# Kernel optimization log

Measured on AMD Instinct MI355X. Metric: run time of the kernel, lower is better.

The kernel has to match this reference:

```python
import jax, jax.numpy as jnp
import numpy as np

B, S, D_IN, D_OUT = 8, 2048, 512, 512

def setup_inputs() -> dict:
    key = jax.random.key(0)
    ks = jax.random.split(key, 10)
    s = 1.0 / np.sqrt(D_IN)
    return {
        "Q": jax.random.normal(ks[0], (B, S, D_IN), jnp.float32),
        "K": jax.random.normal(ks[1], (B, S, D_IN), jnp.float32),
        "V": jax.random.normal(ks[2], (B, S, D_IN), jnp.float32),
        "attn_mask": jax.random.normal(ks[3], (B, S, S), jnp.float32),
        "Wq": jax.random.normal(ks[4], (D_IN, D_OUT), jnp.float32) * s,
        "bq": jnp.zeros((D_OUT,), jnp.float32),
        "Wk": jax.random.normal(ks[5], (D_IN, D_OUT), jnp.float32) * s,
        "bk": jnp.zeros((D_OUT,), jnp.float32),
        "Wv": jax.random.normal(ks[6], (D_IN, D_OUT), jnp.float32) * s,
        "bv": jnp.zeros((D_OUT,), jnp.float32),
    }

def reference(Q, K, V, attn_mask, Wq, bq, Wk, bk, Wv, bv):
    # separate QKV projections
    q_s = jnp.einsum('bsd,de->bse', Q, Wq) + bq
    k_s = jnp.einsum('bsd,de->bse', K, Wk) + bk
    v_s = jnp.einsum('bsd,de->bse', V, Wv) + bv
    # scaled dot-product; note: source scales by sqrt(d_in)
    scale = 1.0 / np.sqrt(Q.shape[-1]).astype(np.float32)
    scores = jnp.einsum('bqe,bke->bqk', q_s, k_s) * scale + attn_mask
    attn = jax.nn.softmax(scores, axis=-1)
    return jnp.einsum('bqk,bke->bqe', attn, v_s)
```

## Files before the change

### kernel.cpp

```cpp
#include <hip/hip_runtime.h>


typedef __bf16 bf16x8 __attribute__((ext_vector_type(8)));
typedef float f32x4 __attribute__((ext_vector_type(4)));

__device__ inline unsigned short f2bf(float x) {
  union { float f; unsigned u; } c; c.f = x;
  unsigned u = c.u;
  return (unsigned short)((u + 0x7fffu + ((u >> 16) & 1u)) >> 16);
}

__device__ inline void load_lds16(const void* g, void* lds) {
  __builtin_amdgcn_global_load_lds(
      (__attribute__((address_space(1))) void*)(g),
      (__attribute__((address_space(3))) void*)(lds),
      16, 0, 0);
}

__global__ __launch_bounds__(256) void cvt4(const float4* __restrict__ src,
                                            ushort4* __restrict__ dst, int n4) {
  int i = blockIdx.x * 256 + threadIdx.x;
  if (i < n4) {
    float4 f = src[i];
    ushort4 o;
    o.x = f2bf(f.x); o.y = f2bf(f.y); o.z = f2bf(f.z); o.w = f2bf(f.w);
    dst[i] = o;
  }
}

__global__ void wtrans(const float* __restrict__ W, unsigned short* __restrict__ Wt) {
  __shared__ float t[32][33];
  const int x = threadIdx.x, y = threadIdx.y;
  const int n0 = blockIdx.x * 32, k0 = blockIdx.y * 32;
#pragma unroll
  for (int j = 0; j < 32; j += 8) t[y + j][x] = W[(size_t)(k0 + y + j) * 512 + n0 + x];
  __syncthreads();
#pragma unroll
  for (int j = 0; j < 32; j += 8)
    Wt[(size_t)(n0 + y + j) * 512 + k0 + x] = f2bf(t[x][y + j]);
}

enum { EPI_PROJ = 0, EPI_SCORES = 1, EPI_PV = 2 };

template <int EPI, int BN>
__global__ __launch_bounds__(256) void gemm_bt(
    const unsigned short* __restrict__ A, size_t sA, int lda,
    const unsigned short* __restrict__ B, size_t sB, int ldb,
    void* __restrict__ Cv, size_t sC, int ldc, int K,
    const float* __restrict__ b0, const float* __restrict__ b1,
    const float* __restrict__ b2, unsigned short* __restrict__ VT,
    const float* __restrict__ mask, float scale, float* __restrict__ Lsum) {
  constexpr int NF = BN / 32;
  __shared__ unsigned short As[128 * 64];
  __shared__ unsigned short Bs[BN * 64];

  const int tid = threadIdx.x;
  const int wave = tid >> 6, lane = tid & 63;
  const int z = blockIdx.z;
  const int m0 = blockIdx.y * 128, n0 = blockIdx.x * BN;

  const unsigned short* Ab = A + (size_t)z * sA;
  const unsigned short* Bb = B + (size_t)z * sB;

  const int wr = wave >> 1, wc = wave & 1;
  const int quad = lane >> 4, c16 = lane & 15;
  const int srow8 = lane >> 3;
  const int sslot = ((lane & 7) ^ srow8) * 8;

  f32x4 acc[4][NF] = {};

  if constexpr (EPI == EPI_SCORES) {
    const float* mb = mask + (size_t)z * 2048 * 2048;
    const float invs = 1.0f / scale;
#pragma unroll
    for (int fr = 0; fr < 4; ++fr)
#pragma unroll
      for (int fc = 0; fc < NF; ++fc)
#pragma unroll
        for (int r = 0; r < 4; ++r)
          acc[fr][fc][r] =
              mb[(size_t)(m0 + wr * 64 + fr * 16 + quad * 4 + r) * 2048 +
                 (n0 + wc * (BN / 2) + fc * 16 + c16)] * invs;
  }

  auto stage = [&](int kt) {
#pragma unroll
    for (int i = 0; i < 4; ++i) {
      const int inst = wave * 4 + i;
      const int row = inst * 8 + srow8;
      load_lds16(Ab + (size_t)(m0 + row) * lda + kt + sslot, &As[inst * 512]);
    }
#pragma unroll
    for (int i = 0; i < BN / 32; ++i) {
      const int inst = wave * (BN / 32) + i;
      const int row = inst * 8 + srow8;
      load_lds16(Bb + (size_t)(n0 + row) * ldb + kt + sslot, &Bs[inst * 512]);
    }
  };

  auto compute = [&]() {
#pragma unroll
    for (int ks = 0; ks < 2; ++ks) {
      bf16x8 af[4], bf[NF];
#pragma unroll
      for (int i = 0; i < 4; ++i) {
        const int row = wr * 64 + i * 16 + c16;
        const int slot = (ks * 4 + quad) ^ (row & 7);
        af[i] = *(const bf16x8*)&As[row * 64 + slot * 8];
      }
#pragma unroll
      for (int j = 0; j < NF; ++j) {
        const int row = wc * (BN / 2) + j * 16 + c16;
        const int slot = (ks * 4 + quad) ^ (row & 7);
        bf[j] = *(const bf16x8*)&Bs[row * 64 + slot * 8];
      }
#pragma unroll
      for (int i = 0; i < 4; ++i)
#pragma unroll
        for (int j = 0; j < NF; ++j)
          acc[i][j] = __builtin_amdgcn_mfma_f32_16x16x32_bf16(af[i], bf[j], acc[i][j], 0, 0, 0);
    }
  };

  if constexpr (EPI == EPI_SCORES) {
#pragma unroll
    for (int it = 0; it < 8; ++it) {
      __syncthreads();
      stage(it * 64);
      __syncthreads();
      compute();
    }
  } else {
    for (int kt = 0; kt < K; kt += 64) {
      __syncthreads();
      stage(kt);
      __syncthreads();
      compute();
    }
  }

#pragma unroll
  for (int fr = 0; fr < 4; ++fr) {
    const int rbase = m0 + wr * 64 + fr * 16 + quad * 4;
    if constexpr (EPI == EPI_PROJ) {
#pragma unroll
      for (int fc = 0; fc < NF; ++fc) {
        const int col = n0 + wc * (BN / 2) + fc * 16 + c16;
        const float bias = (z == 0 ? b0 : (z == 1 ? b1 : b2))[col];
        if (z < 2) {
          unsigned short* C = (unsigned short*)Cv + (size_t)z * sC;
#pragma unroll
          for (int r = 0; r < 4; ++r)
            C[(size_t)(rbase + r) * ldc + col] = f2bf(acc[fr][fc][r] + bias);
        } else {
          const int b = rbase >> 11, s = rbase & 2047;
          ushort4 p;
          p.x = f2bf(acc[fr][fc][0] + bias);
          p.y = f2bf(acc[fr][fc][1] + bias);
          p.z = f2bf(acc[fr][fc][2] + bias);
          p.w = f2bf(acc[fr][fc][3] + bias);
          *(ushort4*)(VT + ((size_t)b * 512 + col) * 2048 + s) = p;
        }
      }
    } else if constexpr (EPI == EPI_SCORES) {
      unsigned short* P = (unsigned short*)Cv + (size_t)z * sC;
      float rs[4] = {0.f, 0.f, 0.f, 0.f};
#pragma unroll
      for (int fc = 0; fc < NF; ++fc) {
        const int col = n0 + wc * (BN / 2) + fc * 16 + c16;
#pragma unroll
        for (int r = 0; r < 4; ++r) {
          const float e = __expf(acc[fr][fc][r] * scale);
          P[(size_t)(rbase + r) * ldc + col] = f2bf(e);
          rs[r] += e;
        }
      }
#pragma unroll
      for (int r = 0; r < 4; ++r) {
#pragma unroll
        for (int off = 1; off < 16; off <<= 1) rs[r] += __shfl_xor(rs[r], off);
      }
      if (c16 == 0) {
#pragma unroll
        for (int r = 0; r < 4; ++r)
          atomicAdd(&Lsum[(size_t)z * 2048 + rbase + r], rs[r]);
      }
    } else {
      float* C = (float*)Cv + (size_t)z * sC;
      float inv[4];
#pragma unroll
      for (int r = 0; r < 4; ++r) inv[r] = 1.0f / Lsum[(size_t)z * 2048 + rbase + r];
#pragma unroll
      for (int fc = 0; fc < NF; ++fc) {
        const int col = n0 + wc * (BN / 2) + fc * 16 + c16;
#pragma unroll
        for (int r = 0; r < 4; ++r)
          C[(size_t)(rbase + r) * ldc + col] = acc[fr][fc][r] * inv[r];
      }
    }
  }
}

extern "C" void kernel_launch(void* const* d_in, const int* in_sizes, int n_in,
                              void* d_out, int out_size, void* d_ws, size_t ws_size,
                              hipStream_t stream) {
  const float* Q    = (const float*)d_in[0];
  const float* Kin  = (const float*)d_in[1];
  const float* V    = (const float*)d_in[2];
  const float* mask = (const float*)d_in[3];
  const float* Wq   = (const float*)d_in[4];
  const float* bq   = (const float*)d_in[5];
  const float* Wk   = (const float*)d_in[6];
  const float* bk   = (const float*)d_in[7];
  const float* Wv   = (const float*)d_in[8];
  const float* bv   = (const float*)d_in[9];
  float* out = (float*)d_out;

  const size_t TOKD = (size_t)16384 * 512;

  unsigned short* WT = (unsigned short*)d_ws;
  unsigned short* QS = WT + 3 * 512 * 512;
  unsigned short* KS = QS + TOKD;
  unsigned short* VT = KS + TOKD;
  unsigned short* P  = VT + TOKD;
  float* Lsum = (float*)(P + (size_t)8 * 2048 * 2048);
  unsigned short* QB = (unsigned short*)(Lsum + 16384);

  const float scale = 0.044194173824159216f;

  const int n4 = (int)(TOKD / 4);
  cvt4<<<n4 / 256, 256, 0, stream>>>((const float4*)Q,   (ushort4*)QB, n4);
  cvt4<<<n4 / 256, 256, 0, stream>>>((const float4*)Kin, (ushort4*)(QB + TOKD), n4);
  cvt4<<<n4 / 256, 256, 0, stream>>>((const float4*)V,   (ushort4*)(QB + 2 * TOKD), n4);

  dim3 wtb(32, 8);
  wtrans<<<dim3(16, 16), wtb, 0, stream>>>(Wq, WT);
  wtrans<<<dim3(16, 16), wtb, 0, stream>>>(Wk, WT + 262144);
  wtrans<<<dim3(16, 16), wtb, 0, stream>>>(Wv, WT + 524288);

  hipMemsetAsync(Lsum, 0, 16384 * sizeof(float), stream);

  gemm_bt<EPI_PROJ, 128><<<dim3(4, 128, 3), 256, 0, stream>>>(
      QB, TOKD, 512, WT, 262144, 512, (void*)QS, TOKD, 512, 512,
      bq, bk, bv, VT, nullptr, 0.f, nullptr);

  gemm_bt<EPI_SCORES, 128><<<dim3(16, 16, 8), 256, 0, stream>>>(
      QS, (size_t)2048 * 512, 512,
      KS, (size_t)2048 * 512, 512,
      (void*)P, (size_t)2048 * 2048, 2048, 512,
      nullptr, nullptr, nullptr, nullptr, mask, scale, Lsum);

  gemm_bt<EPI_PV, 64><<<dim3(8, 16, 8), 256, 0, stream>>>(
      P, (size_t)2048 * 2048, 2048,
      VT, (size_t)512 * 2048, 2048,
      (void*)out, (size_t)2048 * 512, 512, 2048,
      nullptr, nullptr, nullptr, nullptr, nullptr, 0.f, Lsum);
}
```

Measured before the change: 465.9 us.

## Use 256-row double-buffered 512-thread GEMM for scores and PV stages

Adds a new gemm256 kernel with 256xBN tiles, 8 waves per block and double-buffered LDS staging, so the next K-tile loads while the current one computes with one barrier per iteration. The scores and PV GEMMs now use it, and the projection GEMM keeps the old kernel with its scores/PV paths removed. Larger tiles raise data reuse per LDS load. They also increase LDS (up to 128KB per block for scores) and register use, and with fewer blocks per grid this can lower occupancy and CU fill.

```diff
diff --git a/kernel.cpp b/kernel.cpp
--- a/kernel.cpp
+++ b/kernel.cpp
@@ -48,8 +48,7 @@
     const unsigned short* __restrict__ B, size_t sB, int ldb,
     void* __restrict__ Cv, size_t sC, int ldc, int K,
     const float* __restrict__ b0, const float* __restrict__ b1,
-    const float* __restrict__ b2, unsigned short* __restrict__ VT,
-    const float* __restrict__ mask, float scale, float* __restrict__ Lsum) {
+    const float* __restrict__ b2, unsigned short* __restrict__ VT) {
   constexpr int NF = BN / 32;
   __shared__ unsigned short As[128 * 64];
   __shared__ unsigned short Bs[BN * 64];
@@ -69,20 +68,6 @@
 
   f32x4 acc[4][NF] = {};
 
-  if constexpr (EPI == EPI_SCORES) {
-    const float* mb = mask + (size_t)z * 2048 * 2048;
-    const float invs = 1.0f / scale;
-#pragma unroll
-    for (int fr = 0; fr < 4; ++fr)
-#pragma unroll
-      for (int fc = 0; fc < NF; ++fc)
-#pragma unroll
-        for (int r = 0; r < 4; ++r)
-          acc[fr][fc][r] =
-              mb[(size_t)(m0 + wr * 64 + fr * 16 + quad * 4 + r) * 2048 +
-                 (n0 + wc * (BN / 2) + fc * 16 + c16)] * invs;
-  }
-
   auto stage = [&](int kt) {
 #pragma unroll
     for (int i = 0; i < 4; ++i) {
@@ -122,52 +107,144 @@
     }
   };
 
-  if constexpr (EPI == EPI_SCORES) {
-#pragma unroll
-    for (int it = 0; it < 8; ++it) {
-      __syncthreads();
-      stage(it * 64);
-      __syncthreads();
-      compute();
-    }
-  } else {
-    for (int kt = 0; kt < K; kt += 64) {
-      __syncthreads();
-      stage(kt);
-      __syncthreads();
-      compute();
-    }
+  for (int kt = 0; kt < K; kt += 64) {
+    __syncthreads();
+    stage(kt);
+    __syncthreads();
+    compute();
   }
 
 #pragma unroll
   for (int fr = 0; fr < 4; ++fr) {
     const int rbase = m0 + wr * 64 + fr * 16 + quad * 4;
-    if constexpr (EPI == EPI_PROJ) {
-#pragma unroll
-      for (int fc = 0; fc < NF; ++fc) {
-        const int col = n0 + wc * (BN / 2) + fc * 16 + c16;
-        const float bias = (z == 0 ? b0 : (z == 1 ? b1 : b2))[col];
-        if (z < 2) {
-          unsigned short* C = (unsigned short*)Cv + (size_t)z * sC;
-#pragma unroll
-          for (int r = 0; r < 4; ++r)
-            C[(size_t)(rbase + r) * ldc + col] = f2bf(acc[fr][fc][r] + bias);
-        } else {
-          const int b = rbase >> 11, s = rbase & 2047;
-          ushort4 p;
-          p.x = f2bf(acc[fr][fc][0] + bias);
-          p.y = f2bf(acc[fr][fc][1] + bias);
-          p.z = f2bf(acc[fr][fc][2] + bias);
-          p.w = f2bf(acc[fr][fc][3] + bias);
-          *(ushort4*)(VT + ((size_t)b * 512 + col) * 2048 + s) = p;
-        }
-      }
-    } else if constexpr (EPI == EPI_SCORES) {
+#pragma unroll
+    for (int fc = 0; fc < NF; ++fc) {
+      const int col = n0 + wc * (BN / 2) + fc * 16 + c16;
+      const float bias = (z == 0 ? b0 : (z == 1 ? b1 : b2))[col];
+      if (z < 2) {
+        unsigned short* C = (unsigned short*)Cv + (size_t)z * sC;
+#pragma unroll
+        for (int r = 0; r < 4; ++r)
+          C[(size_t)(rbase + r) * ldc + col] = f2bf(acc[fr][fc][r] + bias);
+      } else {
+        const int b = rbase >> 11, s = rbase & 2047;
+        ushort4 p;
+        p.x = f2bf(acc[fr][fc][0] + bias);
+        p.y = f2bf(acc[fr][fc][1] + bias);
+        p.z = f2bf(acc[fr][fc][2] + bias);
+        p.w = f2bf(acc[fr][fc][3] + bias);
+        *(ushort4*)(VT + ((size_t)b * 512 + col) * 2048 + s) = p;
+      }
+    }
+  }
+}
+
+template <int EPI, int BN>
+__global__ __launch_bounds__(512, 2) void gemm256(
+    const unsigned short* __restrict__ A, size_t sA, int lda,
+    const unsigned short* __restrict__ B, size_t sB, int ldb,
+    void* __restrict__ Cv, size_t sC, int ldc, int K,
+    const float* __restrict__ mask, float scale, float* __restrict__ Lsum) {
+  constexpr int WCOL = BN / 4;
+  constexpr int NF = WCOL / 16;
+  __shared__ unsigned short As[2][256 * 64];
+  __shared__ unsigned short Bs[2][BN * 64];
+
+  const int tid = threadIdx.x;
+  const int wave = tid >> 6, lane = tid & 63;
+  const int z = blockIdx.z;
+  const int m0 = blockIdx.y * 256, n0 = blockIdx.x * BN;
+
+  const unsigned short* Ab = A + (size_t)z * sA;
+  const unsigned short* Bb = B + (size_t)z * sB;
+
+  const int wr = wave >> 2, wc = wave & 3;
+  const int quad = lane >> 4, c16 = lane & 15;
+  const int srow8 = lane >> 3;
+  const int sslot = ((lane & 7) ^ srow8) * 8;
+
+  f32x4 acc[8][NF] = {};
+
+  if constexpr (EPI == EPI_SCORES) {
+    const float* mb = mask + (size_t)z * 2048 * 2048;
+    const float invs = 1.0f / scale;
+#pragma unroll
+    for (int fr = 0; fr < 8; ++fr)
+#pragma unroll
+      for (int fc = 0; fc < NF; ++fc)
+#pragma unroll
+        for (int r = 0; r < 4; ++r)
+          acc[fr][fc][r] =
+              mb[(size_t)(m0 + wr * 128 + fr * 16 + quad * 4 + r) * 2048 +
+                 (n0 + wc * WCOL + fc * 16 + c16)] * invs;
+  }
+
+  auto stage = [&](int kt, int b) {
+#pragma unroll
+    for (int i = 0; i < 4; ++i) {
+      const int inst = wave * 4 + i;
+      const int row = inst * 8 + srow8;
+      load_lds16(Ab + (size_t)(m0 + row) * lda + kt + sslot, &As[b][inst * 512]);
+    }
+#pragma unroll
+    for (int i = 0; i < BN / 64; ++i) {
+      const int inst = wave * (BN / 64) + i;
+      const int row = inst * 8 + srow8;
+      load_lds16(Bb + (size_t)(n0 + row) * ldb + kt + sslot, &Bs[b][inst * 512]);
+    }
+  };
+
+  auto compute = [&](int b) {
+#pragma unroll
+    for (int ks = 0; ks < 2; ++ks) {
+      bf16x8 af[8], bf[NF];
+#pragma unroll
+      for (int i = 0; i < 8; ++i) {
+        const int row = wr * 128 + i * 16 + c16;
+        const int slot = (ks * 4 + quad) ^ (row & 7);
+        af[i] = *(const bf16x8*)&As[b][row * 64 + slot * 8];
+      }
+#pragma unroll
+      for (int j = 0; j < NF; ++j) {
+        const int row = wc * WCOL + j * 16 + c16;
+        const int slot = (ks * 4 + quad) ^ (row & 7);
+        bf[j] = *(const bf16x8*)&Bs[b][row * 64 + slot * 8];
+      }
+#pragma unroll
+      for (int i = 0; i < 8; ++i)
+#pragma unroll
+        for (int j = 0; j < NF; ++j)
+          acc[i][j] = __builtin_amdgcn_mfma_f32_16x16x32_bf16(af[i], bf[j], acc[i][j], 0, 0, 0);
+    }
+  };
+
+  stage(0, 0);
+  __syncthreads();
+  if constexpr (EPI == EPI_SCORES) {
+#pragma unroll
+    for (int t = 0; t < 8; ++t) {
+      if (t < 7) stage((t + 1) * 64, (t + 1) & 1);
+      compute(t & 1);
+      __syncthreads();
+    }
+  } else {
+    const int nt = K >> 6;
+    for (int t = 0; t < nt; ++t) {
+      if (t + 1 < nt) stage((t + 1) * 64, (t + 1) & 1);
+      compute(t & 1);
+      __syncthreads();
+    }
+  }
+
+#pragma unroll
+  for (int fr = 0; fr < 8; ++fr) {
+    const int rbase = m0 + wr * 128 + fr * 16 + quad * 4;
+    if constexpr (EPI == EPI_SCORES) {
       unsigned short* P = (unsigned short*)Cv + (size_t)z * sC;
       float rs[4] = {0.f, 0.f, 0.f, 0.f};
 #pragma unroll
       for (int fc = 0; fc < NF; ++fc) {
-        const int col = n0 + wc * (BN / 2) + fc * 16 + c16;
+        const int col = n0 + wc * WCOL + fc * 16 + c16;
 #pragma unroll
         for (int r = 0; r < 4; ++r) {
           const float e = __expf(acc[fr][fc][r] * scale);
@@ -192,7 +269,7 @@
       for (int r = 0; r < 4; ++r) inv[r] = 1.0f / Lsum[(size_t)z * 2048 + rbase + r];
 #pragma unroll
       for (int fc = 0; fc < NF; ++fc) {
-        const int col = n0 + wc * (BN / 2) + fc * 16 + c16;
+        const int col = n0 + wc * WCOL + fc * 16 + c16;
 #pragma unroll
         for (int r = 0; r < 4; ++r)
           C[(size_t)(rbase + r) * ldc + col] = acc[fr][fc][r] * inv[r];
@@ -242,17 +319,17 @@
 
   gemm_bt<EPI_PROJ, 128><<<dim3(4, 128, 3), 256, 0, stream>>>(
       QB, TOKD, 512, WT, 262144, 512, (void*)QS, TOKD, 512, 512,
-      bq, bk, bv, VT, nullptr, 0.f, nullptr);
-
-  gemm_bt<EPI_SCORES, 128><<<dim3(16, 16, 8), 256, 0, stream>>>(
+      bq, bk, bv, VT);
+
+  gemm256<EPI_SCORES, 256><<<dim3(8, 8, 8), 512, 0, stream>>>(
       QS, (size_t)2048 * 512, 512,
       KS, (size_t)2048 * 512, 512,
       (void*)P, (size_t)2048 * 2048, 2048, 512,
-      nullptr, nullptr, nullptr, nullptr, mask, scale, Lsum);
-
-  gemm_bt<EPI_PV, 64><<<dim3(8, 16, 8), 256, 0, stream>>>(
+      mask, scale, Lsum);
+
+  gemm256<EPI_PV, 128><<<dim3(4, 8, 8), 512, 0, stream>>>(
       P, (size_t)2048 * 2048, 2048,
       VT, (size_t)512 * 2048, 2048,
       (void*)out, (size_t)2048 * 512, 512, 2048,
-      nullptr, nullptr, nullptr, nullptr, nullptr, 0.f, Lsum);
-}
+      nullptr, 0.f, Lsum);
+}
```

Measured after the change: 460.6 us. Within noise of the previous version (-1.1%).
